# Optimization experiments

Measured on AMD Instinct MI355X. Metric: run time of the kernel, lower is better.

The kernel has to match this reference:

```python
import jax, jax.numpy as jnp
import numpy as np

EMBED = 1024
HEADS = 16
GQA_GROUPS = 2
KV_HEADS = HEADS // GQA_GROUPS  # 8
HEAD_DIM = EMBED // HEADS       # 64
ALIBI_ALPHA = 1.0
START_I = 0
N, S = 2, 2048


def setup_inputs() -> dict:
    key = jax.random.key(0)
    ks = jax.random.split(key, 6)
    x = jax.random.normal(ks[0], (N, S, EMBED), dtype=jnp.float32)
    sc = 1.0 / np.sqrt(EMBED)
    Wq = jax.random.normal(ks[1], (HEADS * HEAD_DIM, EMBED), dtype=jnp.float32) * sc
    Wk = jax.random.normal(ks[2], (KV_HEADS * HEAD_DIM, EMBED), dtype=jnp.float32) * sc
    Wv = jax.random.normal(ks[3], (KV_HEADS * HEAD_DIM, EMBED), dtype=jnp.float32) * sc
    Wo = jax.random.normal(ks[4], (EMBED, HEADS * HEAD_DIM), dtype=jnp.float32) * sc
    bo = jax.random.normal(ks[5], (EMBED,), dtype=jnp.float32) * 0.01
    return {"x": x, "Wq": Wq, "Wk": Wk, "Wv": Wv, "Wo": Wo, "bo": bo}


def _alibi_bias(q_len, k_len):
    # slopes[i] = 2**(-alpha*(i+start)) for i in 1..heads  -> shape (1,H,1,1)
    i = jnp.arange(1, HEADS + 1, dtype=jnp.float32)
    slopes = jnp.exp2(-ALIBI_ALPHA * (i + START_I)).reshape(1, HEADS, 1, 1)
    t_q = jnp.arange(q_len, dtype=jnp.float32)
    t_k = jnp.arange(k_len, dtype=jnp.float32)
    dist = jnp.abs(t_q[:, None] - t_k[None, :])  # (Q,K), symmetric (non-causal ALiBi)
    return -dist[None, None] * slopes            # (1,H,Q,K)


def reference(x, Wq, Wk, Wv, Wo, bo):
    n, s, _ = x.shape
    q = (x @ Wq.T).reshape(n, s, HEADS, HEAD_DIM)      # nqhd
    k = (x @ Wk.T).reshape(n, s, KV_HEADS, HEAD_DIM)   # nkhd (kv heads)
    v = (x @ Wv.T).reshape(n, s, KV_HEADS, HEAD_DIM)
    # GQA: repeat_interleave kv heads along head dim
    k = jnp.repeat(k, GQA_GROUPS, axis=2)
    v = jnp.repeat(v, GQA_GROUPS, axis=2)
    energy = jnp.einsum("nqhd,nkhd->nhqk", q, k)
    energy = energy + _alibi_bias(s, s)
    # NOTE: original divides (energy + bias) by sqrt(head_dim) inside softmax
    attn = jax.nn.softmax(energy / jnp.sqrt(jnp.float32(HEAD_DIM)), axis=-1)
    out = jnp.einsum("nhqk,nkhd->nqhd", attn, v).reshape(n, s, HEADS * HEAD_DIM)
    return out @ Wo.T + bo
```

## Files before the change

kernel.cpp:

```cpp
#include <hip/hip_runtime.h>

typedef _Float16 f16;
typedef f16 f16x8 __attribute__((ext_vector_type(8)));
typedef f16 f16x4 __attribute__((ext_vector_type(4)));
typedef float f32x4 __attribute__((ext_vector_type(4)));
typedef float f32x16 __attribute__((ext_vector_type(16)));
typedef unsigned uint4v __attribute__((ext_vector_type(4)));

#define GLL(g, l) __builtin_amdgcn_global_load_lds((const __attribute__((address_space(1))) void*)(g), (__attribute__((address_space(3))) void*)(l), 16, 0, 0)

__global__ __launch_bounds__(256) void cvt_all(
    const float* __restrict__ x, const float* __restrict__ wq, const float* __restrict__ wk,
    const float* __restrict__ wv, const float* __restrict__ wo,
    f16* __restrict__ xh, f16* __restrict__ wqh, f16* __restrict__ wkh,
    f16* __restrict__ wvh, f16* __restrict__ woh)
{
  int i = blockIdx.x * 256 + threadIdx.x;
  const float4* src; f16x4* dst; int off;
  if (i < 1048576)      { src = (const float4*)x;  dst = (f16x4*)xh;  off = i; }
  else if (i < 1310720) { src = (const float4*)wq; dst = (f16x4*)wqh; off = i - 1048576; }
  else if (i < 1441792) { src = (const float4*)wk; dst = (f16x4*)wkh; off = i - 1310720; }
  else if (i < 1572864) { src = (const float4*)wv; dst = (f16x4*)wvh; off = i - 1441792; }
  else                  { src = (const float4*)wo; dst = (f16x4*)woh; off = i - 1572864; }
  float4 v = src[off];
  f16x4 hv; hv[0] = (f16)v.x; hv[1] = (f16)v.y; hv[2] = (f16)v.z; hv[3] = (f16)v.w;
  dst[off] = hv;
}

template<int MODE>
__global__ __launch_bounds__(256) void gemm_k(
    const f16* __restrict__ A, const f16* __restrict__ B0, const f16* __restrict__ B1,
    f16* __restrict__ Qb, f16* __restrict__ Kb,
    const float* __restrict__ bo, float* __restrict__ Co)
{
  __shared__ __align__(16) f16 Ah[2][4096];
  __shared__ __align__(16) f16 Bh[2][4096];
  const int tid = threadIdx.x;
  const int bm = blockIdx.x & 31, bn = blockIdx.x >> 5;
  const f16* Bp;
  if (MODE == 0) {
    if (bn < 8)  Bp = B0 + (size_t)bn * 131072;
    else         Bp = B1 + (size_t)(bn - 8) * 131072;
  } else {
    Bp = B0 + (size_t)bn * 131072;
  }
  const f16* Ap = A + (size_t)bm * 131072;

  const int w = tid >> 6, lane = tid & 63, lr = lane & 15, lg = lane >> 4;
  const int wr = w >> 1, wc = w & 1;

  auto stage = [&](int b, int kt) {
#pragma unroll
    for (int i = 0; i < 2; ++i) {
      int o = tid * 16 + i * 4096;
      int row = o >> 6, colb = o & 63;
      GLL((const char*)Ap + (size_t)row * 2048 + kt * 64 + colb, (char*)&Ah[b][0] + o);
      GLL((const char*)Bp + (size_t)row * 2048 + kt * 64 + colb, (char*)&Bh[b][0] + o);
    }
  };

  f32x4 acc[4][4] = {};

  stage(0, 0);
  for (int kt = 0; kt < 32; ++kt) {
    const int cur = kt & 1;
    __syncthreads();
    if (kt < 31) stage(cur ^ 1, kt + 1);
    f16x8 af[4], bf[4];
#pragma unroll
    for (int mi = 0; mi < 4; ++mi)
      af[mi] = *(const f16x8*)((const char*)&Ah[cur][0] + (wr * 64 + mi * 16 + lr) * 64 + lg * 16);
#pragma unroll
    for (int ni = 0; ni < 4; ++ni)
      bf[ni] = *(const f16x8*)((const char*)&Bh[cur][0] + (wc * 64 + ni * 16 + lr) * 64 + lg * 16);
#pragma unroll
    for (int mi = 0; mi < 4; ++mi)
#pragma unroll
      for (int ni = 0; ni < 4; ++ni)
        acc[mi][ni] = __builtin_amdgcn_mfma_f32_16x16x32_f16(af[mi], bf[ni], acc[mi][ni], 0, 0, 0);
    __syncthreads();
  }

  const float C1 = 0.18033688011112042f;
#pragma unroll
  for (int mi = 0; mi < 4; ++mi) {
#pragma unroll
    for (int ni = 0; ni < 4; ++ni) {
      const int ncol = bn * 128 + wc * 64 + ni * 16 + lr;
#pragma unroll
      for (int j = 0; j < 4; ++j) {
        const int m = bm * 128 + wr * 64 + mi * 16 + lg * 4 + j;
        const float v = acc[mi][ni][j];
        if (MODE == 0) {
          const int nb = m >> 11, s = m & 2047;
          if (ncol < 1024) {
            const int hh = ncol >> 6, d = ncol & 63;
            Qb[(((size_t)(nb * 16 + hh)) * 2048 + s) * 64 + d] = (f16)(v * C1);
          } else {
            const int kh = (ncol - 1024) >> 6, d = ncol & 63;
            Kb[(((size_t)(nb * 8 + kh)) * 2048 + s) * 64 + d] = (f16)v;
          }
        } else {
          Co[(size_t)m * 1024 + ncol] = v + bo[ncol];
        }
      }
    }
  }
}

__global__ __launch_bounds__(256) void gemm_vt(
    const f16* __restrict__ A,
    const f16* __restrict__ B,
    f16* __restrict__ C)
{
  __shared__ __align__(16) f16 Ah[2][2048];
  __shared__ __align__(16) f16 Bh[2][4096];
  const int tid = threadIdx.x;
  const int bm = blockIdx.x & 7, bn = blockIdx.x >> 3;
  const f16* Ap = A + (size_t)bm * 65536;
  const f16* Bp = B + (size_t)bn * 131072;
  const int w = tid >> 6, lane = tid & 63, lr = lane & 15, lg = lane >> 4;
  const int wr = w >> 1, wc = w & 1;

  auto stage = [&](int b, int kt) {
    {
      int o = tid * 16;
      int row = o >> 6, colb = o & 63;
      GLL((const char*)Ap + (size_t)row * 2048 + kt * 64 + colb, (char*)&Ah[b][0] + o);
    }
#pragma unroll
    for (int i = 0; i < 2; ++i) {
      int o = tid * 16 + i * 4096;
      int row = o >> 6, colb = o & 63;
      GLL((const char*)Bp + (size_t)row * 2048 + kt * 64 + colb, (char*)&Bh[b][0] + o);
    }
  };

  f32x4 acc[2][4] = {};
  stage(0, 0);
  for (int kt = 0; kt < 32; ++kt) {
    const int cur = kt & 1;
    __syncthreads();
    if (kt < 31) stage(cur ^ 1, kt + 1);
    f16x8 af[2], bf[4];
#pragma unroll
    for (int mi = 0; mi < 2; ++mi)
      af[mi] = *(const f16x8*)((const char*)&Ah[cur][0] + (wr * 32 + mi * 16 + lr) * 64 + lg * 16);
#pragma unroll
    for (int ni = 0; ni < 4; ++ni)
      bf[ni] = *(const f16x8*)((const char*)&Bh[cur][0] + (wc * 64 + ni * 16 + lr) * 64 + lg * 16);
#pragma unroll
    for (int mi = 0; mi < 2; ++mi)
#pragma unroll
      for (int ni = 0; ni < 4; ++ni)
        acc[mi][ni] = __builtin_amdgcn_mfma_f32_16x16x32_f16(af[mi], bf[ni], acc[mi][ni], 0, 0, 0);
    __syncthreads();
  }

#pragma unroll
  for (int mi = 0; mi < 2; ++mi)
#pragma unroll
    for (int ni = 0; ni < 4; ++ni) {
      const int ncol = bn * 128 + wc * 64 + ni * 16 + lr;
#pragma unroll
      for (int j = 0; j < 4; ++j) {
        const int m = bm * 64 + wr * 32 + mi * 16 + lg * 4 + j;
        C[(size_t)m * 4096 + ncol] = (f16)acc[mi][ni][j];
      }
    }
}

__global__ __launch_bounds__(512, 2) void attn_k(
    const f16* __restrict__ Qb, const f16* __restrict__ Kb, const f16* __restrict__ VTb,
    f16* __restrict__ Ob)
{
  __shared__ __align__(16) char SMEM[65536];

  const int tid = threadIdx.x, w = tid >> 6, l = tid & 63;
  const int lq = l & 31, hi = l >> 5;
  const int half = w >> 2, g = w & 3;
  const int qt = blockIdx.x, nh = blockIdx.y;
  const int n = nh >> 4, h = nh & 15, kvh = h >> 1;
  const int qb = qt * 128;
  const int qhat = qb + g * 32 + lq;

  const f16* Qp = Qb + ((size_t)(n * 16 + h) * 2048 + qhat) * 64;
  f16x8 qf[4];
#pragma unroll
  for (int cd = 0; cd < 4; ++cd)
    qf[cd] = *(const f16x8*)(Qp + cd * 16 + hi * 8);

  const char* Kg = (const char*)(Kb + (size_t)(n * 8 + kvh) * 2048 * 64);
  const char* Vg = (const char*)(VTb + (size_t)kvh * 64 * 4096 + (size_t)n * 2048);

  const int t256 = tid & 255;
  const int s0 = t256 * 16, s1 = s0 + 4096;
  const int r0 = s0 >> 7, c0 = ((s0 >> 4) & 7) ^ (r0 & 7);
  const int r1 = s1 >> 7, c1 = ((s1 >> 4) & 7) ^ (r1 & 7);
  char* KB0 = SMEM + half * 32768;

  auto stageK = [&](int buf, int tb) {
    char* d = KB0 + buf * 16384;
    GLL(Kg + (size_t)(tb * 64 + r0) * 128 + c0 * 16, d + s0);
    GLL(Kg + (size_t)(tb * 64 + r1) * 128 + c1 * 16, d + s1);
  };
  auto stageV = [&](int buf, int tb) {
    char* d = KB0 + buf * 16384 + 8192;
    GLL(Vg + (size_t)r0 * 8192 + tb * 128 + c0 * 16, d + s0);
    GLL(Vg + (size_t)r1 * 8192 + tb * 128 + c1 * 16, d + s1);
  };

  f32x16 oacc[2] = {};
  f32x16 lacc = {};
  float p[2][16];
  float m_r = -1e30f;
  const float C1 = 0.18033688011112042f;
  const float slt = exp2f(-(float)(h + 1)) * C1;
  const float qpos = (float)qhat;

  f16x8 ones;
#pragma unroll
  for (int i = 0; i < 8; ++i) ones[i] = (f16)1.0f;

  stageK(0, half * 16); stageV(0, half * 16);

  for (int t = 0; t < 16; ++t) {
    const int cur = t & 1;
    const int tb = half * 16 + t;
    __syncthreads();
    if (t < 15) { stageK(cur ^ 1, tb + 1); stageV(cur ^ 1, tb + 1); }
    const char* Kl = KB0 + cur * 16384;
    const char* Vl = Kl + 8192;

#pragma unroll
    for (int kt = 0; kt < 2; ++kt) {
      f32x16 c = {};
#pragma unroll
      for (int cd = 0; cd < 4; ++cd) {
        const int row = kt * 32 + lq;
        f16x8 kf = *(const f16x8*)(Kl + row * 128 + (((2 * cd + hi) ^ (row & 7)) * 16));
        c = __builtin_amdgcn_mfma_f32_32x32x16_f16(kf, qf[cd], c, 0, 0, 0);
      }
      const float kb0 = (float)(tb * 64 + kt * 32 + 4 * hi);
#pragma unroll
      for (int r = 0; r < 16; ++r) {
        float kpos = kb0 + (float)((r & 3) + 8 * (r >> 2));
        p[kt][r] = fmaf(-fabsf(qpos - kpos), slt, c[r]);
      }
    }

    float pmax = p[0][0];
#pragma unroll
    for (int kt = 0; kt < 2; ++kt)
#pragma unroll
      for (int r = 0; r < 16; ++r) pmax = fmaxf(pmax, p[kt][r]);
    pmax = fmaxf(pmax, __shfl_xor(pmax, 32));

    if (!__all(pmax - m_r <= 8.0f)) {
      float mn = fmaxf(m_r, pmax);
      float sc = __builtin_amdgcn_exp2f(m_r - mn);
      m_r = mn;
#pragma unroll
      for (int dt = 0; dt < 2; ++dt)
#pragma unroll
        for (int r = 0; r < 16; ++r) oacc[dt][r] *= sc;
#pragma unroll
      for (int r = 0; r < 16; ++r) lacc[r] *= sc;
    }
#pragma unroll
    for (int kt = 0; kt < 2; ++kt)
#pragma unroll
      for (int r = 0; r < 16; ++r)
        p[kt][r] = __builtin_amdgcn_exp2f(p[kt][r] - m_r);

    f16x8 pf[4];
#pragma unroll
    for (int c2 = 0; c2 < 4; ++c2) {
      const int T = c2 >> 1, e = c2 & 1;
      unsigned w0 = __builtin_bit_cast(unsigned, __builtin_amdgcn_cvt_pkrtz(p[T][8 * e + 0], p[T][8 * e + 1]));
      unsigned w2 = __builtin_bit_cast(unsigned, __builtin_amdgcn_cvt_pkrtz(p[T][8 * e + 4], p[T][8 * e + 5]));
      unsigned w1 = __builtin_bit_cast(unsigned, __builtin_amdgcn_cvt_pkrtz(p[T][8 * e + 2], p[T][8 * e + 3]));
      unsigned w3 = __builtin_bit_cast(unsigned, __builtin_amdgcn_cvt_pkrtz(p[T][8 * e + 6], p[T][8 * e + 7]));
      asm volatile("v_permlane32_swap_b32 %0, %1" : "+v"(w0), "+v"(w2));
      asm volatile("v_permlane32_swap_b32 %0, %1" : "+v"(w1), "+v"(w3));
      uint4v pu; pu.x = w0; pu.y = w1; pu.z = w2; pu.w = w3;
      pf[c2] = __builtin_bit_cast(f16x8, pu);
    }

#pragma unroll
    for (int dt = 0; dt < 2; ++dt) {
#pragma unroll
      for (int ck = 0; ck < 4; ++ck) {
        const int row = dt * 32 + lq;
        f16x8 vf = *(const f16x8*)(Vl + row * 128 + (((2 * ck + hi) ^ (row & 7)) * 16));
        oacc[dt] = __builtin_amdgcn_mfma_f32_32x32x16_f16(vf, pf[ck], oacc[dt], 0, 0, 0);
      }
    }
#pragma unroll
    for (int ck = 0; ck < 4; ++ck)
      lacc = __builtin_amdgcn_mfma_f32_32x32x16_f16(ones, pf[ck], lacc, 0, 0, 0);
  }

  const float l_r = lacc[0];

  float* Xo = (float*)SMEM;
  float* Xm = (float*)(SMEM + 33792);
  float* Xl = (float*)(SMEM + 34304);
  f16* Ot = (f16*)SMEM;

  __syncthreads();
  if (half) {
#pragma unroll
    for (int dt = 0; dt < 2; ++dt)
#pragma unroll
      for (int r = 0; r < 16; ++r) {
        const int d = dt * 32 + (r & 3) + 8 * (r >> 2) + 4 * hi;
        Xo[(g * 32 + lq) * 66 + d] = oacc[dt][r];
      }
    if (!hi) { Xm[g * 32 + lq] = m_r; Xl[g * 32 + lq] = l_r; }
  }
  __syncthreads();
  float fin[2][16];
  if (!half) {
    const float m1 = Xm[g * 32 + lq], l1 = Xl[g * 32 + lq];
    const float mm = fmaxf(m_r, m1);
    const float a0 = __builtin_amdgcn_exp2f(m_r - mm);
    const float a1 = __builtin_amdgcn_exp2f(m1 - mm);
    const float linv = 1.0f / (l_r * a0 + l1 * a1);
#pragma unroll
    for (int dt = 0; dt < 2; ++dt)
#pragma unroll
      for (int r = 0; r < 16; ++r) {
        const int d = dt * 32 + (r & 3) + 8 * (r >> 2) + 4 * hi;
        fin[dt][r] = (oacc[dt][r] * a0 + Xo[(g * 32 + lq) * 66 + d] * a1) * linv;
      }
  }
  __syncthreads();
  if (!half) {
#pragma unroll
    for (int dt = 0; dt < 2; ++dt)
#pragma unroll
      for (int r = 0; r < 16; ++r) {
        const int d = dt * 32 + (r & 3) + 8 * (r >> 2) + 4 * hi;
        Ot[(g * 32 + lq) * 72 + d] = (f16)fin[dt][r];
      }
  }
  __syncthreads();
  {
    const int q = tid >> 2, seg = tid & 3;
    const f16* src = &Ot[q * 72 + seg * 16];
    f16* dst = Ob + (size_t)(n * 2048 + qb + q) * 1024 + h * 64 + seg * 16;
    *(f16x8*)(dst) = *(const f16x8*)(src);
    *(f16x8*)(dst + 8) = *(const f16x8*)(src + 8);
  }
}

extern "C" void kernel_launch(void* const* d_in, const int* in_sizes, int n_in,
                              void* d_out, int out_size, void* d_ws, size_t ws_size,
                              hipStream_t stream) {
  const float* x  = (const float*)d_in[0];
  const float* Wq = (const float*)d_in[1];
  const float* Wk = (const float*)d_in[2];
  const float* Wv = (const float*)d_in[3];
  const float* Wo = (const float*)d_in[4];
  const float* bo = (const float*)d_in[5];

  char* ws = (char*)d_ws;
  f16* xh  = (f16*)(ws);
  f16* wqh = (f16*)(ws + 8388608);
  f16* wkh = (f16*)(ws + 10485760);
  f16* wvh = (f16*)(ws + 11534336);
  f16* woh = (f16*)(ws + 12582912);
  f16* Qb  = (f16*)(ws + 14680064);
  f16* Kb  = (f16*)(ws + 23068672);
  f16* VTb = (f16*)(ws + 27262976);
  f16* Ob  = (f16*)(ws + 31457280);

  cvt_all<<<7168, 256, 0, stream>>>(x, Wq, Wk, Wv, Wo, xh, wqh, wkh, wvh, woh);
  gemm_k<0><<<384, 256, 0, stream>>>(xh, wqh, wkh, Qb, Kb, nullptr, nullptr);
  gemm_vt<<<256, 256, 0, stream>>>(wvh, xh, VTb);
  attn_k<<<dim3(16, 32), 512, 0, stream>>>(Qb, Kb, VTb, Ob);
  gemm_k<1><<<256, 256, 0, stream>>>(Ob, woh, nullptr, nullptr, nullptr, bo, (float*)d_out);
}
```

Baseline: 144.8 us.

## Split attention KV range four ways and read K/V directly from global memory

The attention kernel now handles 64 queries per block instead of 128, with four wave pairs each covering a quarter of the key range. It drops the LDS double-buffered K/V staging and its per-iteration barriers in favour of direct global loads per lane. The four partial softmax results are merged through shared memory. It also switches the row max to a tree reduction. The grid doubles, giving more blocks and no in-loop syncs, but K/V traffic now goes through the caches without LDS reuse and may raise global load latency.

After: 209.4 us. 44.6% more time.

```diff
diff --git a/kernel.cpp b/kernel.cpp
--- a/kernel.cpp
+++ b/kernel.cpp
@@ -174,15 +174,15 @@
     const f16* __restrict__ Qb, const f16* __restrict__ Kb, const f16* __restrict__ VTb,
     f16* __restrict__ Ob)
 {
-  __shared__ __align__(16) char SMEM[65536];
+  __shared__ __align__(16) char SMEM[52224];
 
   const int tid = threadIdx.x, w = tid >> 6, l = tid & 63;
   const int lq = l & 31, hi = l >> 5;
-  const int half = w >> 2, g = w & 3;
+  const int qg = w & 1, kvq = w >> 1;
   const int qt = blockIdx.x, nh = blockIdx.y;
   const int n = nh >> 4, h = nh & 15, kvh = h >> 1;
-  const int qb = qt * 128;
-  const int qhat = qb + g * 32 + lq;
+  const int qb = qt * 64;
+  const int qhat = qb + qg * 32 + lq;
 
   const f16* Qp = Qb + ((size_t)(n * 16 + h) * 2048 + qhat) * 64;
   f16x8 qf[4];
@@ -190,25 +190,8 @@
   for (int cd = 0; cd < 4; ++cd)
     qf[cd] = *(const f16x8*)(Qp + cd * 16 + hi * 8);
 
-  const char* Kg = (const char*)(Kb + (size_t)(n * 8 + kvh) * 2048 * 64);
-  const char* Vg = (const char*)(VTb + (size_t)kvh * 64 * 4096 + (size_t)n * 2048);
-
-  const int t256 = tid & 255;
-  const int s0 = t256 * 16, s1 = s0 + 4096;
-  const int r0 = s0 >> 7, c0 = ((s0 >> 4) & 7) ^ (r0 & 7);
-  const int r1 = s1 >> 7, c1 = ((s1 >> 4) & 7) ^ (r1 & 7);
-  char* KB0 = SMEM + half * 32768;
-
-  auto stageK = [&](int buf, int tb) {
-    char* d = KB0 + buf * 16384;
-    GLL(Kg + (size_t)(tb * 64 + r0) * 128 + c0 * 16, d + s0);
-    GLL(Kg + (size_t)(tb * 64 + r1) * 128 + c1 * 16, d + s1);
-  };
-  auto stageV = [&](int buf, int tb) {
-    char* d = KB0 + buf * 16384 + 8192;
-    GLL(Vg + (size_t)r0 * 8192 + tb * 128 + c0 * 16, d + s0);
-    GLL(Vg + (size_t)r1 * 8192 + tb * 128 + c1 * 16, d + s1);
-  };
+  const char* Krow = (const char*)(Kb + (size_t)(n * 8 + kvh) * 2048 * 64) + lq * 128 + hi * 16;
+  const char* Vrow = (const char*)(VTb + (size_t)kvh * 64 * 4096 + (size_t)n * 2048) + (size_t)lq * 8192 + hi * 16;
 
   f32x16 oacc[2] = {};
   f32x16 lacc = {};
@@ -222,23 +205,15 @@
 #pragma unroll
   for (int i = 0; i < 8; ++i) ones[i] = (f16)1.0f;
 
-  stageK(0, half * 16); stageV(0, half * 16);
-
-  for (int t = 0; t < 16; ++t) {
-    const int cur = t & 1;
-    const int tb = half * 16 + t;
-    __syncthreads();
-    if (t < 15) { stageK(cur ^ 1, tb + 1); stageV(cur ^ 1, tb + 1); }
-    const char* Kl = KB0 + cur * 16384;
-    const char* Vl = Kl + 8192;
+  for (int t = 0; t < 8; ++t) {
+    const int tb = kvq * 8 + t;
 
 #pragma unroll
     for (int kt = 0; kt < 2; ++kt) {
       f32x16 c = {};
 #pragma unroll
       for (int cd = 0; cd < 4; ++cd) {
-        const int row = kt * 32 + lq;
-        f16x8 kf = *(const f16x8*)(Kl + row * 128 + (((2 * cd + hi) ^ (row & 7)) * 16));
+        f16x8 kf = *(const f16x8*)(Krow + (size_t)(tb * 64 + kt * 32) * 128 + cd * 32);
         c = __builtin_amdgcn_mfma_f32_32x32x16_f16(kf, qf[cd], c, 0, 0, 0);
       }
       const float kb0 = (float)(tb * 64 + kt * 32 + 4 * hi);
@@ -249,12 +224,14 @@
       }
     }
 
-    float pmax = p[0][0];
-#pragma unroll
-    for (int kt = 0; kt < 2; ++kt)
-#pragma unroll
-      for (int r = 0; r < 16; ++r) pmax = fmaxf(pmax, p[kt][r]);
-    pmax = fmaxf(pmax, __shfl_xor(pmax, 32));
+    float mx[16];
+#pragma unroll
+    for (int r = 0; r < 16; ++r) mx[r] = fmaxf(p[0][r], p[1][r]);
+#pragma unroll
+    for (int st = 8; st; st >>= 1)
+#pragma unroll
+      for (int r = 0; r < st; ++r) mx[r] = fmaxf(mx[r], mx[r + st]);
+    float pmax = fmaxf(mx[0], __shfl_xor(mx[0], 32));
 
     if (!__all(pmax - m_r <= 8.0f)) {
       float mn = fmaxf(m_r, pmax);
@@ -291,8 +268,7 @@
     for (int dt = 0; dt < 2; ++dt) {
 #pragma unroll
       for (int ck = 0; ck < 4; ++ck) {
-        const int row = dt * 32 + lq;
-        f16x8 vf = *(const f16x8*)(Vl + row * 128 + (((2 * ck + hi) ^ (row & 7)) * 16));
+        f16x8 vf = *(const f16x8*)(Vrow + (size_t)dt * 32 * 8192 + tb * 128 + ck * 32);
         oacc[dt] = __builtin_amdgcn_mfma_f32_32x32x16_f16(vf, pf[ck], oacc[dt], 0, 0, 0);
       }
     }
@@ -301,57 +277,61 @@
       lacc = __builtin_amdgcn_mfma_f32_32x32x16_f16(ones, pf[ck], lacc, 0, 0, 0);
   }
 
-  const float l_r = lacc[0];
+  float l_r = lacc[0];
 
   float* Xo = (float*)SMEM;
-  float* Xm = (float*)(SMEM + 33792);
-  float* Xl = (float*)(SMEM + 34304);
+  float* Xm = (float*)(SMEM + 50688);
+  float* Xl = (float*)(SMEM + 51456);
   f16* Ot = (f16*)SMEM;
+  const int base = qg * 32 + lq;
 
   __syncthreads();
-  if (half) {
+  if (kvq) {
+    const int set = kvq - 1;
 #pragma unroll
     for (int dt = 0; dt < 2; ++dt)
 #pragma unroll
       for (int r = 0; r < 16; ++r) {
         const int d = dt * 32 + (r & 3) + 8 * (r >> 2) + 4 * hi;
-        Xo[(g * 32 + lq) * 66 + d] = oacc[dt][r];
-      }
-    if (!hi) { Xm[g * 32 + lq] = m_r; Xl[g * 32 + lq] = l_r; }
+        Xo[(set * 64 + base) * 66 + d] = oacc[dt][r];
+      }
+    if (!hi) { Xm[set * 64 + base] = m_r; Xl[set * 64 + base] = l_r; }
   }
   __syncthreads();
-  float fin[2][16];
-  if (!half) {
-    const float m1 = Xm[g * 32 + lq], l1 = Xl[g * 32 + lq];
-    const float mm = fmaxf(m_r, m1);
-    const float a0 = __builtin_amdgcn_exp2f(m_r - mm);
-    const float a1 = __builtin_amdgcn_exp2f(m1 - mm);
-    const float linv = 1.0f / (l_r * a0 + l1 * a1);
+  if (!kvq) {
+#pragma unroll
+    for (int set = 0; set < 3; ++set) {
+      const float m1 = Xm[set * 64 + base], l1 = Xl[set * 64 + base];
+      const float mm = fmaxf(m_r, m1);
+      const float a0 = __builtin_amdgcn_exp2f(m_r - mm);
+      const float a1 = __builtin_amdgcn_exp2f(m1 - mm);
+      m_r = mm; l_r = l_r * a0 + l1 * a1;
+#pragma unroll
+      for (int dt = 0; dt < 2; ++dt)
+#pragma unroll
+        for (int r = 0; r < 16; ++r) {
+          const int d = dt * 32 + (r & 3) + 8 * (r >> 2) + 4 * hi;
+          oacc[dt][r] = oacc[dt][r] * a0 + Xo[(set * 64 + base) * 66 + d] * a1;
+        }
+    }
+  }
+  __syncthreads();
+  if (!kvq) {
+    const float linv = 1.0f / l_r;
 #pragma unroll
     for (int dt = 0; dt < 2; ++dt)
 #pragma unroll
       for (int r = 0; r < 16; ++r) {
         const int d = dt * 32 + (r & 3) + 8 * (r >> 2) + 4 * hi;
-        fin[dt][r] = (oacc[dt][r] * a0 + Xo[(g * 32 + lq) * 66 + d] * a1) * linv;
-      }
-  }
-  __syncthreads();
-  if (!half) {
-#pragma unroll
-    for (int dt = 0; dt < 2; ++dt)
-#pragma unroll
-      for (int r = 0; r < 16; ++r) {
-        const int d = dt * 32 + (r & 3) + 8 * (r >> 2) + 4 * hi;
-        Ot[(g * 32 + lq) * 72 + d] = (f16)fin[dt][r];
+        Ot[base * 72 + d] = (f16)(oacc[dt][r] * linv);
       }
   }
   __syncthreads();
   {
-    const int q = tid >> 2, seg = tid & 3;
-    const f16* src = &Ot[q * 72 + seg * 16];
-    f16* dst = Ob + (size_t)(n * 2048 + qb + q) * 1024 + h * 64 + seg * 16;
+    const int q = tid >> 3, seg = tid & 7;
+    const f16* src = &Ot[q * 72 + seg * 8];
+    f16* dst = Ob + (size_t)(n * 2048 + qb + q) * 1024 + h * 64 + seg * 8;
     *(f16x8*)(dst) = *(const f16x8*)(src);
-    *(f16x8*)(dst + 8) = *(const f16x8*)(src + 8);
   }
 }
 
@@ -379,6 +359,6 @@
   cvt_all<<<7168, 256, 0, stream>>>(x, Wq, Wk, Wv, Wo, xh, wqh, wkh, wvh, woh);
   gemm_k<0><<<384, 256, 0, stream>>>(xh, wqh, wkh, Qb, Kb, nullptr, nullptr);
   gemm_vt<<<256, 256, 0, stream>>>(wvh, xh, VTb);
-  attn_k<<<dim3(16, 32), 512, 0, stream>>>(Qb, Kb, VTb, Ob);
+  attn_k<<<dim3(32, 32), 512, 0, stream>>>(Qb, Kb, VTb, Ob);
   gemm_k<1><<<256, 256, 0, stream>>>(Ob, woh, nullptr, nullptr, nullptr, bo, (float*)d_out);
 }
```
